# Kernel tuning notes

Hardware: AMD Instinct MI355X
Metric: run time of the kernel (lower is better)

Reference implementation:

```python
import jax, jax.numpy as jnp
import numpy as np

B, H, T, D = 2, 8, 2048, 64
STATE = H * D  # 512

def setup_inputs() -> dict:
    key = jax.random.key(0)
    kq, kk, kv, kw, kl = jax.random.split(key, 5)
    q = jax.random.normal(kq, (B * H, T, D), jnp.float32)
    k = jax.random.normal(kk, (B * H, T, D), jnp.float32)
    v = jax.random.normal(kv, (B * H, T, D), jnp.float32)
    # causal position mask: True = masked (future positions)
    position_mask = jnp.triu(jnp.ones((T, T), dtype=bool), 1)
    # per-batch source lengths in [T//2, T]; True = padding (masked)
    lengths = jax.random.randint(kl, (B,), T // 2, T + 1)
    src_length_mask = jnp.arange(T)[None, :] >= lengths[:, None]
    W_merge = jax.random.normal(kw, (STATE, STATE), jnp.float32) / np.sqrt(STATE)
    return {"q": q, "k": k, "v": v, "position_mask": position_mask,
            "src_length_mask": src_length_mask, "W_merge": W_merge}

def reference(q, k, v, position_mask, src_length_mask, W_merge):
    bb, n_dest, d = q.shape              # bb = B*H
    n_batch = src_length_mask.shape[0]
    n_heads = bb // n_batch
    scale = 1.0 / np.sqrt(d)
    # [bb, T_dest, T_src] full score matrix (as in the torch bmm)
    logits = jnp.einsum('btd,bsd->bts', q, k) * scale
    logits = logits.reshape(n_batch, n_heads, n_dest, -1)
    logits = jnp.where(position_mask[None, None], -jnp.inf, logits)
    logits = jnp.where(src_length_mask[:, None, None, :], -jnp.inf, logits)
    scores = jax.nn.softmax(logits, axis=-1).reshape(bb, n_dest, -1)
    # dropout p=0 (eval) -> identity
    out = jnp.einsum('bts,bsd->btd', scores, v)
    out = out.reshape(n_batch, n_heads, n_dest, d).transpose(0, 2, 1, 3)
    out = out.reshape(n_batch, n_dest, n_heads * d)
    return out @ W_merge.T  # bias-free Linear merge
```

## Files before the change

kernel.cpp:

```cpp
#include <hip/hip_runtime.h>

#define TT 2048
#define DD 64
#define NSTATE 512

typedef __attribute__((ext_vector_type(8))) short short8;
typedef __attribute__((ext_vector_type(4))) short short4v;
typedef __attribute__((ext_vector_type(4))) float f4;

__device__ __forceinline__ short f2bf(float x) {
  union { float f; unsigned u; } c; c.f = x;
  unsigned r = (c.u + 0x7FFFu + ((c.u >> 16) & 1u)) >> 16;
  return (short)r;
}

__device__ __forceinline__ bool mask_at(const void* p, bool u8, int idx) {
  return u8 ? (((const unsigned char*)p)[idx] != 0)
            : (((const int*)p)[idx] != 0);
}

__device__ __forceinline__ void gld16(const void* g, void* l) {
  __builtin_amdgcn_global_load_lds(
      (const __attribute__((address_space(1))) void*)g,
      (__attribute__((address_space(3))) void*)l, 16, 0, 0);
}

__global__ __launch_bounds__(256)
void prep_kernel(const float* __restrict__ k, const float* __restrict__ v,
                 const float* __restrict__ W, const void* __restrict__ posmask,
                 const void* __restrict__ srcmask,
                 unsigned short* __restrict__ Wb, unsigned short* __restrict__ Kimg,
                 unsigned short* __restrict__ VTimg, int* __restrict__ lenbuf) {
  const int bidx = blockIdx.x;
  const int tid = threadIdx.x;
  if (bidx < 512) {
    const int bh = bidx >> 5, tile = bidx & 31;
    const float* kp = k + (bh * TT + tile * 64) * DD;
    unsigned short* dst = Kimg + (bh * 32 + tile) * 4096;
#pragma unroll
    for (int t2 = 0; t2 < 2; ++t2) {
      int j = tid + t2 * 256;
      int c8 = j >> 6, r6 = j & 63;
      int kb = c8 >> 1, cc = c8 & 1, qd = r6 >> 4, klo = r6 & 15;
      int key = kb * 16 + klo, dg = cc * 4 + qd;
      f4 a0 = *(const f4*)(kp + key * DD + dg * 8);
      f4 a1 = *(const f4*)(kp + key * DD + dg * 8 + 4);
      short8 o;
      o[0]=f2bf(a0[0]); o[1]=f2bf(a0[1]); o[2]=f2bf(a0[2]); o[3]=f2bf(a0[3]);
      o[4]=f2bf(a1[0]); o[5]=f2bf(a1[1]); o[6]=f2bf(a1[2]); o[7]=f2bf(a1[3]);
      *(short8*)(dst + j * 8) = o;
    }
    __shared__ float Vt[64][65];
    const float* vp = v + (bh * TT + tile * 64) * DD;
    {
      int key = tid >> 2, c0 = (tid & 3) * 16;
#pragma unroll
      for (int i = 0; i < 4; ++i) {
        f4 x = *(const f4*)(vp + key * DD + c0 + i * 4);
        Vt[key][c0 + i * 4 + 0] = x[0];
        Vt[key][c0 + i * 4 + 1] = x[1];
        Vt[key][c0 + i * 4 + 2] = x[2];
        Vt[key][c0 + i * 4 + 3] = x[3];
      }
    }
    __syncthreads();
    unsigned short* vd = VTimg + (bh * 32 + tile) * 5120;
#pragma unroll
    for (int t2 = 0; t2 < 3; ++t2) {
      int j = tid + t2 * 256;
      if (j < 640) {
        int d = j / 10, sc = j - d * 10;
        short8 o = (short8){0,0,0,0,0,0,0,0};
        if (sc < 8) {
#pragma unroll
          for (int i = 0; i < 8; ++i) o[i] = f2bf(Vt[sc * 8 + i][d]);
        }
        *(short8*)(vd + d * 80 + sc * 8) = o;
      }
    }
  } else if (bidx < 768) {
    int i = ((bidx - 512) * 256 + tid) * 4;
    f4 x = *(const f4*)(W + i);
    short4v o;
    o[0]=f2bf(x[0]); o[1]=f2bf(x[1]); o[2]=f2bf(x[2]); o[3]=f2bf(x[3]);
    *(short4v*)(Wb + i) = o;
  } else {
    const int wv = tid >> 6, lane = tid & 63;
    if (wv < 2) {
      const bool u8 = (((const unsigned char*)posmask)[1] != 0);
      int pos = 1024 + lane * 16;
      bool m1 = mask_at(srcmask, u8, wv * TT + pos);
      unsigned long long bal = __ballot(m1);
      int cur = bal ? (1024 + (__ffsll((unsigned long long)bal) - 1) * 16) : 2048;
      int prev = cur - 16;
      bool m2 = false;
      if (lane < 16) {
        int pos2 = prev + 1 + lane;
        m2 = (pos2 < TT) ? mask_at(srcmask, u8, wv * TT + pos2) : true;
      }
      unsigned long long bal2 = __ballot(m2);
      int len = prev + 1 + (__ffsll((unsigned long long)bal2) - 1);
      if (lane == 0) lenbuf[wv] = len;
    }
  }
}

__global__ __launch_bounds__(128)
void attn_kernel(const float* __restrict__ q, const unsigned short* __restrict__ Kimg,
                 const unsigned short* __restrict__ VTimg,
                 const int* __restrict__ lenbuf, unsigned short* __restrict__ merged) {
  const int bid = blockIdx.x;
  const int bh = bid & 15;
  const int qraw = bid >> 4;
  const int qt = (qraw & 1) ? (63 - (qraw >> 1)) : (qraw >> 1);
  const int b = bh >> 3, h = bh & 7;
  const int tid = threadIdx.x;
  const int w = tid >> 6, lane = tid & 63;
  const int lane_lo = lane & 15, quad = lane >> 4;
  const int q0 = qt * 32 + w * 16;
  const int len = lenbuf[b];
  const int n_st = min((qt >> 1) + 1, (len + 63) >> 6);

  __shared__ __attribute__((aligned(16))) unsigned short Klds[2][4096];
  __shared__ __attribute__((aligned(16))) unsigned short Vlds[2][5120];

  short8 qf[2];
  {
    const float* qrow = q + ((bh * TT) + q0 + lane_lo) * DD;
#pragma unroll
    for (int c = 0; c < 2; ++c) {
      int d0 = c * 32 + quad * 8;
      f4 a0 = *(const f4*)(qrow + d0);
      f4 a1 = *(const f4*)(qrow + d0 + 4);
      short8 t;
      t[0]=f2bf(a0[0]*0.125f); t[1]=f2bf(a0[1]*0.125f);
      t[2]=f2bf(a0[2]*0.125f); t[3]=f2bf(a0[3]*0.125f);
      t[4]=f2bf(a1[0]*0.125f); t[5]=f2bf(a1[1]*0.125f);
      t[6]=f2bf(a1[2]*0.125f); t[7]=f2bf(a1[3]*0.125f);
      qf[c] = t;
    }
  }

  float l_lane = 0.f;
  f4 O[4];
#pragma unroll
  for (int d = 0; d < 4; ++d) O[d] = (f4){0.f, 0.f, 0.f, 0.f};

  const char* kbase = (const char*)(Kimg + (size_t)bh * 32 * 4096);
  const char* vbase = (const char*)(VTimg + (size_t)bh * 32 * 5120);

  auto stage = [&](int st, int bufi) {
    const char* ks = kbase + st * 8192 + w * 4096 + lane * 16;
    char* kl = (char*)&Klds[bufi][0] + w * 4096 + lane * 16;
#pragma unroll
    for (int i = 0; i < 4; ++i) gld16(ks + i * 1024, kl + i * 1024);
    const char* vs = vbase + st * 10240 + w * 5120 + lane * 16;
    char* vl = (char*)&Vlds[bufi][0] + w * 5120 + lane * 16;
#pragma unroll
    for (int i = 0; i < 5; ++i) gld16(vs + i * 1024, vl + i * 1024);
  };

  stage(0, 0);
  __syncthreads();

  for (int st = 0; st < n_st; ++st) {
    const int bufc = st & 1;
    if (st + 1 < n_st) stage(st + 1, bufc ^ 1);
    const unsigned short* Kl = Klds[bufc];
    const unsigned short* Vl = Vlds[bufc];
    const int s0 = st * 64;

    f4 ST[4];
#pragma unroll
    for (int sb = 0; sb < 4; ++sb) {
      f4 acc = (f4){0.f, 0.f, 0.f, 0.f};
#pragma unroll
      for (int c = 0; c < 2; ++c) {
        short8 kf = *(const short8*)&Kl[((sb * 2 + c) * 64 + lane) * 8];
        acc = __builtin_amdgcn_mfma_f32_16x16x32_bf16(kf, qf[c], acc, 0, 0, 0);
      }
      ST[sb] = acc;
    }

    const bool edge = (st == (qt >> 1)) || (s0 + 64 > len);
    const int tq = q0 + lane_lo;
    short4v pf[4];
#pragma unroll
    for (int sb = 0; sb < 4; ++sb) {
#pragma unroll
      for (int r = 0; r < 4; ++r) {
        float p = __expf(ST[sb][r]);
        if (edge) {
          int s = s0 + sb * 16 + quad * 4 + r;
          if (s > tq || s >= len) p = 0.f;
        }
        l_lane += p;
        pf[sb][r] = f2bf(p);
      }
    }

#pragma unroll
    for (int db = 0; db < 4; ++db) {
      f4 acc = O[db];
#pragma unroll
      for (int sb = 0; sb < 4; ++sb) {
        short4v vf = *(const short4v*)&Vl[(db * 16 + lane_lo) * 80 + sb * 16 + quad * 4];
        acc = __builtin_amdgcn_mfma_f32_16x16x16bf16_1k(pf[sb], vf, acc, 0, 0, 0);
      }
      O[db] = acc;
    }
    __syncthreads();
  }

  l_lane += __shfl_xor(l_lane, 16);
  l_lane += __shfl_xor(l_lane, 32);
  float inv = 1.0f / l_lane;
  float invr[4];
#pragma unroll
  for (int r = 0; r < 4; ++r) invr[r] = __shfl(inv, quad * 4 + r);
#pragma unroll
  for (int db = 0; db < 4; ++db)
#pragma unroll
    for (int r = 0; r < 4; ++r) {
      int t = q0 + quad * 4 + r;
      merged[((b * TT) + t) * NSTATE + h * DD + db * 16 + lane_lo] =
          (unsigned short)f2bf(O[db][r] * invr[r]);
    }
}

__global__ __launch_bounds__(256)
void merge_kernel(const unsigned short* __restrict__ A,
                  const unsigned short* __restrict__ Wb,
                  float* __restrict__ out) {
  __shared__ __attribute__((aligned(16))) unsigned short Wl[64 * 512];
  const int tid = threadIdx.x;
  const int n0 = blockIdx.x * 64, m0 = blockIdx.y * 64;
  {
    int row = tid >> 2, cb = (tid & 3) * 16;
    const unsigned short* src = Wb + (n0 + row) * NSTATE;
#pragma unroll
    for (int j = 0; j < 16; ++j) {
      int c = cb + j;
      int phys = c ^ (row & 7);
      *(short8*)&Wl[row * 512 + phys * 8] = *(const short8*)(src + c * 8);
    }
  }
  __syncthreads();

  const int w = tid >> 6, lane = tid & 63;
  const int lo16 = lane & 15, quad = lane >> 4;
  const int m = m0 + w * 16;
  f4 acc[4];
#pragma unroll
  for (int nf = 0; nf < 4; ++nf) acc[nf] = (f4){0.f, 0.f, 0.f, 0.f};
  const unsigned short* arow = A + (m + lo16) * NSTATE + quad * 8;
#pragma unroll 4
  for (int k0 = 0; k0 < NSTATE; k0 += 32) {
    short8 af = *(const short8*)(arow + k0);
#pragma unroll
    for (int nf = 0; nf < 4; ++nf) {
      int n = nf * 16 + lo16;
      int phys = ((k0 >> 3) + quad) ^ (n & 7);
      short8 bf = *(const short8*)&Wl[n * 512 + phys * 8];
      acc[nf] = __builtin_amdgcn_mfma_f32_16x16x32_bf16(af, bf, acc[nf], 0, 0, 0);
    }
  }
#pragma unroll
  for (int nf = 0; nf < 4; ++nf)
#pragma unroll
    for (int r = 0; r < 4; ++r)
      out[(m + quad * 4 + r) * NSTATE + n0 + nf * 16 + lo16] = acc[nf][r];
}

extern "C" void kernel_launch(void* const* d_in, const int* in_sizes, int n_in,
                              void* d_out, int out_size, void* d_ws, size_t ws_size,
                              hipStream_t stream) {
  (void)in_sizes; (void)n_in; (void)out_size; (void)ws_size;
  const float* q = (const float*)d_in[0];
  const float* k = (const float*)d_in[1];
  const float* v = (const float*)d_in[2];
  const void* posm = d_in[3];
  const void* srcm = d_in[4];
  const float* W = (const float*)d_in[5];
  float* out = (float*)d_out;

  unsigned short* merged = (unsigned short*)d_ws;
  unsigned short* Wb     = merged + 2097152;
  unsigned short* Kimg   = Wb + 262144;
  unsigned short* VTimg  = Kimg + 2097152;
  int* lenbuf = (int*)(VTimg + 2621440);

  prep_kernel<<<dim3(769), dim3(256), 0, stream>>>(k, v, W, posm, srcm,
                                                   Wb, Kimg, VTimg, lenbuf);
  attn_kernel<<<dim3(1024), dim3(128), 0, stream>>>(q, Kimg, VTimg, lenbuf, merged);
  merge_kernel<<<dim3(8, 64), dim3(256), 0, stream>>>(merged, Wb, out);
}
```

Baseline: 139.4 us.

## Load K/V fragments straight to registers, one wave per block

```diff
diff --git a/kernel.cpp b/kernel.cpp
--- a/kernel.cpp
+++ b/kernel.cpp
@@ -19,10 +19,11 @@
             : (((const int*)p)[idx] != 0);
 }
 
-__device__ __forceinline__ void gld16(const void* g, void* l) {
-  __builtin_amdgcn_global_load_lds(
-      (const __attribute__((address_space(1))) void*)g,
-      (__attribute__((address_space(3))) void*)l, 16, 0, 0);
+__device__ __forceinline__ short4v lo4(short8 x) {
+  short4v r; r[0] = x[0]; r[1] = x[1]; r[2] = x[2]; r[3] = x[3]; return r;
+}
+__device__ __forceinline__ short4v hi4(short8 x) {
+  short4v r; r[0] = x[4]; r[1] = x[5]; r[2] = x[6]; r[3] = x[7]; return r;
 }
 
 __global__ __launch_bounds__(256)
@@ -64,19 +65,19 @@
       }
     }
     __syncthreads();
-    unsigned short* vd = VTimg + (bh * 32 + tile) * 5120;
-#pragma unroll
-    for (int t2 = 0; t2 < 3; ++t2) {
+    unsigned short* vd = VTimg + (bh * 32 + tile) * 4096;
+#pragma unroll
+    for (int t2 = 0; t2 < 2; ++t2) {
       int j = tid + t2 * 256;
-      if (j < 640) {
-        int d = j / 10, sc = j - d * 10;
-        short8 o = (short8){0,0,0,0,0,0,0,0};
-        if (sc < 8) {
-#pragma unroll
-          for (int i = 0; i < 8; ++i) o[i] = f2bf(Vt[sc * 8 + i][d]);
-        }
-        *(short8*)(vd + d * 80 + sc * 8) = o;
-      }
+      int d = j >> 3, c8 = j & 7;
+      short8 o;
+#pragma unroll
+      for (int ii = 0; ii < 8; ++ii) {
+        int p = c8 * 8 + ii;
+        int qd = p >> 4, sb = (p >> 2) & 3, r = p & 3;
+        o[ii] = f2bf(Vt[sb * 16 + qd * 4 + r][d]);
+      }
+      *(short8*)(vd + d * 64 + c8 * 8) = o;
     }
   } else if (bidx < 768) {
     int i = ((bidx - 512) * 256 + tid) * 4;
@@ -105,24 +106,20 @@
   }
 }
 
-__global__ __launch_bounds__(128)
+__global__ __launch_bounds__(64, 2)
 void attn_kernel(const float* __restrict__ q, const unsigned short* __restrict__ Kimg,
                  const unsigned short* __restrict__ VTimg,
                  const int* __restrict__ lenbuf, unsigned short* __restrict__ merged) {
-  const int bid = blockIdx.x;
-  const int bh = bid & 15;
-  const int qraw = bid >> 4;
-  const int qt = (qraw & 1) ? (63 - (qraw >> 1)) : (qraw >> 1);
+  const int i = blockIdx.x;
+  const int bh = ((i & 7) << 1) | ((i >> 3) & 1);
+  const int qtr = i >> 4;
+  const int qt = (qtr & 1) ? (127 - (qtr >> 1)) : (qtr >> 1);
   const int b = bh >> 3, h = bh & 7;
-  const int tid = threadIdx.x;
-  const int w = tid >> 6, lane = tid & 63;
+  const int lane = threadIdx.x;
   const int lane_lo = lane & 15, quad = lane >> 4;
-  const int q0 = qt * 32 + w * 16;
+  const int q0 = qt * 16;
   const int len = lenbuf[b];
-  const int n_st = min((qt >> 1) + 1, (len + 63) >> 6);
-
-  __shared__ __attribute__((aligned(16))) unsigned short Klds[2][4096];
-  __shared__ __attribute__((aligned(16))) unsigned short Vlds[2][5120];
+  const int n_st = min((qt >> 2) + 1, (len + 63) >> 6);
 
   short8 qf[2];
   {
@@ -146,47 +143,40 @@
 #pragma unroll
   for (int d = 0; d < 4; ++d) O[d] = (f4){0.f, 0.f, 0.f, 0.f};
 
-  const char* kbase = (const char*)(Kimg + (size_t)bh * 32 * 4096);
-  const char* vbase = (const char*)(VTimg + (size_t)bh * 32 * 5120);
-
-  auto stage = [&](int st, int bufi) {
-    const char* ks = kbase + st * 8192 + w * 4096 + lane * 16;
-    char* kl = (char*)&Klds[bufi][0] + w * 4096 + lane * 16;
-#pragma unroll
-    for (int i = 0; i < 4; ++i) gld16(ks + i * 1024, kl + i * 1024);
-    const char* vs = vbase + st * 10240 + w * 5120 + lane * 16;
-    char* vl = (char*)&Vlds[bufi][0] + w * 5120 + lane * 16;
-#pragma unroll
-    for (int i = 0; i < 5; ++i) gld16(vs + i * 1024, vl + i * 1024);
+  const char* kbase = (const char*)Kimg + (size_t)bh * 262144 + lane * 16;
+  const char* vbase = (const char*)VTimg + (size_t)bh * 262144 +
+                      (lane_lo * 4 + quad) * 32;
+
+  short8 kA[8], kB[8], vA[8], vB[8];
+
+  auto loadK = [&](int st, short8 (&kf)[8]) {
+    const char* p = kbase + st * 8192;
+#pragma unroll
+    for (int j = 0; j < 8; ++j) kf[j] = *(const short8*)(p + j * 1024);
   };
-
-  stage(0, 0);
-  __syncthreads();
-
-  for (int st = 0; st < n_st; ++st) {
-    const int bufc = st & 1;
-    if (st + 1 < n_st) stage(st + 1, bufc ^ 1);
-    const unsigned short* Kl = Klds[bufc];
-    const unsigned short* Vl = Vlds[bufc];
+  auto loadV = [&](int st, short8 (&vf)[8]) {
+    const char* p = vbase + st * 8192;
+#pragma unroll
+    for (int j = 0; j < 4; ++j) {
+      vf[j * 2]     = *(const short8*)(p + j * 2048);
+      vf[j * 2 + 1] = *(const short8*)(p + j * 2048 + 16);
+    }
+  };
+  auto step = [&](int st, const short8 (&kf)[8], const short8 (&vf)[8]) {
     const int s0 = st * 64;
-
     f4 ST[4];
 #pragma unroll
     for (int sb = 0; sb < 4; ++sb) {
       f4 acc = (f4){0.f, 0.f, 0.f, 0.f};
-#pragma unroll
-      for (int c = 0; c < 2; ++c) {
-        short8 kf = *(const short8*)&Kl[((sb * 2 + c) * 64 + lane) * 8];
-        acc = __builtin_amdgcn_mfma_f32_16x16x32_bf16(kf, qf[c], acc, 0, 0, 0);
-      }
+      acc = __builtin_amdgcn_mfma_f32_16x16x32_bf16(kf[sb * 2 + 0], qf[0], acc, 0, 0, 0);
+      acc = __builtin_amdgcn_mfma_f32_16x16x32_bf16(kf[sb * 2 + 1], qf[1], acc, 0, 0, 0);
       ST[sb] = acc;
     }
-
-    const bool edge = (st == (qt >> 1)) || (s0 + 64 > len);
+    const bool edge = (st == (qt >> 2)) || (s0 + 64 > len);
     const int tq = q0 + lane_lo;
     short4v pf[4];
 #pragma unroll
-    for (int sb = 0; sb < 4; ++sb) {
+    for (int sb = 0; sb < 4; ++sb)
 #pragma unroll
       for (int r = 0; r < 4; ++r) {
         float p = __expf(ST[sb][r]);
@@ -197,19 +187,27 @@
         l_lane += p;
         pf[sb][r] = f2bf(p);
       }
-    }
-
 #pragma unroll
     for (int db = 0; db < 4; ++db) {
       f4 acc = O[db];
-#pragma unroll
-      for (int sb = 0; sb < 4; ++sb) {
-        short4v vf = *(const short4v*)&Vl[(db * 16 + lane_lo) * 80 + sb * 16 + quad * 4];
-        acc = __builtin_amdgcn_mfma_f32_16x16x16bf16_1k(pf[sb], vf, acc, 0, 0, 0);
-      }
+      acc = __builtin_amdgcn_mfma_f32_16x16x16bf16_1k(pf[0], lo4(vf[db * 2]),     acc, 0, 0, 0);
+      acc = __builtin_amdgcn_mfma_f32_16x16x16bf16_1k(pf[1], hi4(vf[db * 2]),     acc, 0, 0, 0);
+      acc = __builtin_amdgcn_mfma_f32_16x16x16bf16_1k(pf[2], lo4(vf[db * 2 + 1]), acc, 0, 0, 0);
+      acc = __builtin_amdgcn_mfma_f32_16x16x16bf16_1k(pf[3], hi4(vf[db * 2 + 1]), acc, 0, 0, 0);
       O[db] = acc;
     }
-    __syncthreads();
+  };
+
+  loadK(0, kA); loadV(0, vA);
+  if (n_st > 1) { loadK(1, kB); loadV(1, vB); }
+  int st = 0;
+  while (true) {
+    step(st, kA, vA);
+    ++st; if (st >= n_st) break;
+    if (st + 1 < n_st) { loadK(st + 1, kA); loadV(st + 1, vA); }
+    step(st, kB, vB);
+    ++st; if (st >= n_st) break;
+    if (st + 1 < n_st) { loadK(st + 1, kB); loadV(st + 1, vB); }
   }
 
   l_lane += __shfl_xor(l_lane, 16);
@@ -288,10 +286,10 @@
   unsigned short* Wb     = merged + 2097152;
   unsigned short* Kimg   = Wb + 262144;
   unsigned short* VTimg  = Kimg + 2097152;
-  int* lenbuf = (int*)(VTimg + 2621440);
+  int* lenbuf = (int*)(VTimg + 2097152);
 
   prep_kernel<<<dim3(769), dim3(256), 0, stream>>>(k, v, W, posm, srcm,
                                                    Wb, Kimg, VTimg, lenbuf);
-  attn_kernel<<<dim3(1024), dim3(128), 0, stream>>>(q, Kimg, VTimg, lenbuf, merged);
+  attn_kernel<<<dim3(2048), dim3(64), 0, stream>>>(q, Kimg, VTimg, lenbuf, merged);
   merge_kernel<<<dim3(8, 64), dim3(256), 0, stream>>>(merged, Wb, out);
 }
```

New measurement: 154.2 us. +10.6%, slower.

## Use 64-query tiles with 4 waves, fragment-ordered V image, and MFMA priority

Applied to the files above, without the earlier changes.

```diff
diff --git a/kernel.cpp b/kernel.cpp
--- a/kernel.cpp
+++ b/kernel.cpp
@@ -64,19 +64,22 @@
       }
     }
     __syncthreads();
-    unsigned short* vd = VTimg + (bh * 32 + tile) * 5120;
-#pragma unroll
-    for (int t2 = 0; t2 < 3; ++t2) {
+    unsigned short* vd = VTimg + (bh * 32 + tile) * 4096;
+#pragma unroll
+    for (int t2 = 0; t2 < 2; ++t2) {
       int j = tid + t2 * 256;
-      if (j < 640) {
-        int d = j / 10, sc = j - d * 10;
-        short8 o = (short8){0,0,0,0,0,0,0,0};
-        if (sc < 8) {
-#pragma unroll
-          for (int i = 0; i < 8; ++i) o[i] = f2bf(Vt[sc * 8 + i][d]);
-        }
-        *(short8*)(vd + d * 80 + sc * 8) = o;
-      }
+      int fs = j >> 5;
+      int db = fs >> 2, sb = fs & 3;
+      int jj = j & 31;
+      short8 o;
+#pragma unroll
+      for (int ii = 0; ii < 8; ++ii) {
+        int l = jj * 2 + (ii >> 2), r = ii & 3;
+        int s = sb * 16 + (l >> 4) * 4 + r;
+        int d = db * 16 + (l & 15);
+        o[ii] = f2bf(Vt[s][d]);
+      }
+      *(short8*)(vd + j * 8) = o;
     }
   } else if (bidx < 768) {
     int i = ((bidx - 512) * 256 + tid) * 4;
@@ -105,24 +108,24 @@
   }
 }
 
-__global__ __launch_bounds__(128)
+__global__ __launch_bounds__(256)
 void attn_kernel(const float* __restrict__ q, const unsigned short* __restrict__ Kimg,
                  const unsigned short* __restrict__ VTimg,
                  const int* __restrict__ lenbuf, unsigned short* __restrict__ merged) {
-  const int bid = blockIdx.x;
-  const int bh = bid & 15;
-  const int qraw = bid >> 4;
-  const int qt = (qraw & 1) ? (63 - (qraw >> 1)) : (qraw >> 1);
+  const int i = blockIdx.x;
+  const int bh = ((i & 7) << 1) | ((i >> 3) & 1);
+  const int tr = i >> 4;
+  const int tile = (tr < 16) ? tr : 47 - tr;
   const int b = bh >> 3, h = bh & 7;
   const int tid = threadIdx.x;
   const int w = tid >> 6, lane = tid & 63;
   const int lane_lo = lane & 15, quad = lane >> 4;
-  const int q0 = qt * 32 + w * 16;
+  const int q0 = tile * 64 + w * 16;
   const int len = lenbuf[b];
-  const int n_st = min((qt >> 1) + 1, (len + 63) >> 6);
+  const int n_st = min(tile + 1, (len + 63) >> 6);
 
   __shared__ __attribute__((aligned(16))) unsigned short Klds[2][4096];
-  __shared__ __attribute__((aligned(16))) unsigned short Vlds[2][5120];
+  __shared__ __attribute__((aligned(16))) unsigned short Vlds[2][4096];
 
   short8 qf[2];
   {
@@ -146,18 +149,16 @@
 #pragma unroll
   for (int d = 0; d < 4; ++d) O[d] = (f4){0.f, 0.f, 0.f, 0.f};
 
-  const char* kbase = (const char*)(Kimg + (size_t)bh * 32 * 4096);
-  const char* vbase = (const char*)(VTimg + (size_t)bh * 32 * 5120);
+  const char* kbase = (const char*)Kimg + (size_t)bh * 262144;
+  const char* vbase = (const char*)VTimg + (size_t)bh * 262144;
 
   auto stage = [&](int st, int bufi) {
-    const char* ks = kbase + st * 8192 + w * 4096 + lane * 16;
-    char* kl = (char*)&Klds[bufi][0] + w * 4096 + lane * 16;
-#pragma unroll
-    for (int i = 0; i < 4; ++i) gld16(ks + i * 1024, kl + i * 1024);
-    const char* vs = vbase + st * 10240 + w * 5120 + lane * 16;
-    char* vl = (char*)&Vlds[bufi][0] + w * 5120 + lane * 16;
-#pragma unroll
-    for (int i = 0; i < 5; ++i) gld16(vs + i * 1024, vl + i * 1024);
+    const char* ks = kbase + st * 8192 + w * 2048 + lane * 16;
+    char* kl = (char*)&Klds[bufi][0] + w * 2048 + lane * 16;
+    gld16(ks, kl); gld16(ks + 1024, kl + 1024);
+    const char* vs = vbase + st * 8192 + w * 2048 + lane * 16;
+    char* vl = (char*)&Vlds[bufi][0] + w * 2048 + lane * 16;
+    gld16(vs, vl); gld16(vs + 1024, vl + 1024);
   };
 
   stage(0, 0);
@@ -171,6 +172,7 @@
     const int s0 = st * 64;
 
     f4 ST[4];
+    __builtin_amdgcn_s_setprio(1);
 #pragma unroll
     for (int sb = 0; sb < 4; ++sb) {
       f4 acc = (f4){0.f, 0.f, 0.f, 0.f};
@@ -181,12 +183,13 @@
       }
       ST[sb] = acc;
     }
-
-    const bool edge = (st == (qt >> 1)) || (s0 + 64 > len);
+    __builtin_amdgcn_s_setprio(0);
+
+    const bool edge = (st == tile) || (s0 + 64 > len);
     const int tq = q0 + lane_lo;
     short4v pf[4];
 #pragma unroll
-    for (int sb = 0; sb < 4; ++sb) {
+    for (int sb = 0; sb < 4; ++sb)
 #pragma unroll
       for (int r = 0; r < 4; ++r) {
         float p = __expf(ST[sb][r]);
@@ -197,18 +200,19 @@
         l_lane += p;
         pf[sb][r] = f2bf(p);
       }
-    }
-
+
+    __builtin_amdgcn_s_setprio(1);
 #pragma unroll
     for (int db = 0; db < 4; ++db) {
       f4 acc = O[db];
 #pragma unroll
       for (int sb = 0; sb < 4; ++sb) {
-        short4v vf = *(const short4v*)&Vl[(db * 16 + lane_lo) * 80 + sb * 16 + quad * 4];
+        short4v vf = *(const short4v*)&Vl[(db * 4 + sb) * 256 + lane * 4];
         acc = __builtin_amdgcn_mfma_f32_16x16x16bf16_1k(pf[sb], vf, acc, 0, 0, 0);
       }
       O[db] = acc;
     }
+    __builtin_amdgcn_s_setprio(0);
     __syncthreads();
   }
 
@@ -288,10 +292,10 @@
   unsigned short* Wb     = merged + 2097152;
   unsigned short* Kimg   = Wb + 262144;
   unsigned short* VTimg  = Kimg + 2097152;
-  int* lenbuf = (int*)(VTimg + 2621440);
+  int* lenbuf = (int*)(VTimg + 2097152);
 
   prep_kernel<<<dim3(769), dim3(256), 0, stream>>>(k, v, W, posm, srcm,
                                                    Wb, Kimg, VTimg, lenbuf);
-  attn_kernel<<<dim3(1024), dim3(128), 0, stream>>>(q, Kimg, VTimg, lenbuf, merged);
+  attn_kernel<<<dim3(512), dim3(256), 0, stream>>>(q, Kimg, VTimg, lenbuf, merged);
   merge_kernel<<<dim3(8, 64), dim3(256), 0, stream>>>(merged, Wb, out);
 }
```

Result: faster. 131.5 us (-5.7%).
